# Kernel tuning notes

Hardware: AMD Instinct MI355X
Metric: run time of the kernel (lower is better)

The kernel has to match this reference:

```python
import jax, jax.numpy as jnp
import numpy as np

B, S, D, H, W = 2, 2048, 1024, 16, 128
HD = D // H


def setup_inputs() -> dict:
    key = jax.random.key(0)
    ks = jax.random.split(key, 9)
    s = 1.0 / np.sqrt(D)
    return {
        "x": jax.random.normal(ks[0], (B, S, D), jnp.float32),
        "Wq": jax.random.normal(ks[1], (D, D), jnp.float32) * s,
        "bq": jax.random.normal(ks[2], (D,), jnp.float32) * 0.01,
        "Wk": jax.random.normal(ks[3], (D, D), jnp.float32) * s,
        "bk": jax.random.normal(ks[4], (D,), jnp.float32) * 0.01,
        "Wv": jax.random.normal(ks[5], (D, D), jnp.float32) * s,
        "bv": jax.random.normal(ks[6], (D,), jnp.float32) * 0.01,
        "Wo": jax.random.normal(ks[7], (D, D), jnp.float32) * s,
        "bo": jax.random.normal(ks[8], (D,), jnp.float32) * 0.01,
    }


def reference(x, Wq, bq, Wk, bk, Wv, bv, Wo, bo):
    b, s, d = x.shape
    # projections (torch Linear: x @ W.T + b)
    q = (jnp.einsum('bsd,ed->bse', x, Wq) + bq).reshape(b, s, H, HD).transpose(0, 2, 1, 3)
    k = (jnp.einsum('bsd,ed->bse', x, Wk) + bk).reshape(b, s, H, HD).transpose(0, 2, 1, 3)
    v = (jnp.einsum('bsd,ed->bse', x, Wv) + bv).reshape(b, s, H, HD).transpose(0, 2, 1, 3)
    scores = jnp.einsum('bhqd,bhkd->bhqk', q, k) / jnp.sqrt(jnp.asarray(HD, x.dtype))
    # local band mask: mask[i, j] = 1 iff i - W//2 <= j <= i + W//2
    idx = jnp.arange(s)
    band = jnp.abs(idx[:, None] - idx[None, :]) <= (W // 2)  # [S, S]
    scores = jnp.where(band[None, None], scores, -jnp.inf)
    attn = jax.nn.softmax(scores, axis=-1)  # dropout is identity in eval
    ctx = jnp.einsum('bhqk,bhkd->bqhd', attn, v).reshape(b, s, d)
    out = jnp.einsum('bsd,ed->bse', ctx, Wo) + bo
    return out, attn
```

## Files before the change

### kernel.cpp

```cpp
#include <hip/hip_runtime.h>
#include <math.h>
#include <stdint.h>

typedef _Float16 f16;
typedef f16   f16x8 __attribute__((ext_vector_type(8)));
typedef f16   f16x4 __attribute__((ext_vector_type(4)));
typedef float f32x4 __attribute__((ext_vector_type(4)));

constexpr int Bc = 2, Sc = 2048, Dc = 1024, Hc = 16, HDc = 64;
constexpr size_t PROJ = (size_t)Bc * Sc * Dc;
constexpr size_t WN   = (size_t)Dc * Dc;

__device__ __forceinline__ void gload_lds16(const void* g, void* l) {
    unsigned int off = (unsigned int)(uintptr_t)l;
    auto lp = (__attribute__((address_space(3))) unsigned int*)(uintptr_t)off;
    auto gp = (const __attribute__((address_space(1))) unsigned int*)(uintptr_t)g;
    __builtin_amdgcn_global_load_lds(gp, lp, 16, 0, 0);
}

__device__ __forceinline__ void fill_rows32(float* __restrict__ attn, int grow0, int t) {
    const uint4 z = {0u, 0u, 0u, 0u};
    for (int rr = 0; rr < 32; ++rr) {
        const int gr = grow0 + rr;
        const int i = gr & (Sc - 1);
        const int lo = (i > 64) ? (i - 64) : 0;
        const int a0 = lo & ~31;
        const int hi = (i < Sc - 65) ? (i + 64) : (Sc - 1);
        int a1 = (hi + 32) & ~31; if (a1 > Sc) a1 = Sc;
        uint4* rowp = (uint4*)(attn + (size_t)gr * Sc);
        const int n4L = a0 >> 2;
        const int r0  = a1 >> 2;
        const int tot = n4L + (512 - r0);
        for (int idx = t; idx < tot; idx += 256) {
            const int p = (idx < n4L) ? idx : (r0 + idx - n4L);
            rowp[p] = z;
        }
    }
}

__global__ __launch_bounds__(256)
void pack_all(const float* __restrict__ x,
              const float* __restrict__ w0, const float* __restrict__ w1,
              const float* __restrict__ w2, const float* __restrict__ w3,
              f16* __restrict__ xd, f16* __restrict__ wd, f16* __restrict__ vT) {
    const int bid = blockIdx.x;
    if (bid == 8192) {
        const uint4 z = {0u, 0u, 0u, 0u};
        uint4* pre  = (uint4*)(vT - 256);
        uint4* post = (uint4*)(vT + (size_t)4 * 1024 * 1024);
        const int t = threadIdx.x;
        if (t < 32) pre[t] = z;
        else if (t < 64) post[t - 32] = z;
        return;
    }
    const float* src;
    f16* dst;
    int off4;
    if (bid < 4096) {
        src = x; dst = xd; off4 = bid;
    } else {
        const int wi = (bid - 4096) >> 10;
        const int r  = (bid - 4096) & 1023;
        src = (wi == 0) ? w0 : (wi == 1) ? w1 : (wi == 2) ? w2 : w3;
        dst = wd + (size_t)wi * WN;
        off4 = r;
    }
    const int i = off4 * 256 + threadIdx.x;
    float4 f = ((const float4*)src)[i];
    f16x4 h = {(f16)f.x, (f16)f.y, (f16)f.z, (f16)f.w};
    ((f16x4*)dst)[i] = h;
}

template <typename OutT, bool WITH_FILL>
__global__ __launch_bounds__(256, 3)
void gemm_mega(const f16* __restrict__ A, const f16* __restrict__ W,
               const float* __restrict__ b0, const float* __restrict__ b1,
               const float* __restrict__ b2,
               OutT* __restrict__ o0, OutT* __restrict__ o1, OutT* __restrict__ o2,
               float* __restrict__ fill, int n_ct) {
    constexpr int K = 1024, N = 1024;
    const int bid = blockIdx.x;
    const int t = threadIdx.x;

    int gid = bid;
    if (WITH_FILL) {
        const int g8 = bid >> 3, l8 = bid & 7;
        if (l8 < 3) {
            gid = g8 * 3 + l8;
        } else {
            fill_rows32(fill, (g8 * 5 + (l8 - 3)) * 32, t);
            return;
        }
    }

    __shared__ f16 sA[128 * 32];
    __shared__ f16 sB[128 * 32];

    const int w = t >> 6, l = t & 63, l15 = l & 15, quad = l >> 4;
    const int col_t = gid % n_ct, row_t = gid / n_ct;
    const int row0 = row_t * 128, col0 = col_t * 128;
    const int wr = w >> 1, wc = w & 1;

    f32x4 acc[4][4];
    #pragma unroll
    for (int i = 0; i < 4; ++i)
        #pragma unroll
        for (int j = 0; j < 4; ++j) acc[i][j] = (f32x4){0.f, 0.f, 0.f, 0.f};

    const int arow = t >> 2;
    const int koff = (t & 3) * 8;
    const f16* ga = A + (size_t)(row0 + arow) * K + koff;
    const f16* gb = W + (size_t)(col0 + arow) * K + koff;
    f16* lA1 = sA + w * 512;
    f16* lA2 = sA + 2048 + w * 512;
    f16* lB1 = sB + w * 512;
    f16* lB2 = sB + 2048 + w * 512;

    for (int k0 = 0; k0 < K; k0 += 32) {
        gload_lds16(ga + k0, lA1);
        gload_lds16(ga + (size_t)64 * K + k0, lA2);
        gload_lds16(gb + k0, lB1);
        gload_lds16(gb + (size_t)64 * K + k0, lB2);
        __syncthreads();

        f16x8 af[4], bf[4];
        #pragma unroll
        for (int mi = 0; mi < 4; ++mi)
            af[mi] = *(const f16x8*)&sA[(wr * 64 + mi * 16 + l15) * 32 + quad * 8];
        #pragma unroll
        for (int ni = 0; ni < 4; ++ni)
            bf[ni] = *(const f16x8*)&sB[(wc * 64 + ni * 16 + l15) * 32 + quad * 8];
        #pragma unroll
        for (int mi = 0; mi < 4; ++mi)
            #pragma unroll
            for (int ni = 0; ni < 4; ++ni)
                acc[mi][ni] = __builtin_amdgcn_mfma_f32_16x16x32_f16(af[mi], bf[ni], acc[mi][ni], 0, 0, 0);
        __syncthreads();
    }

    const int ten = col0 >> 10;
    const float* bias = (ten == 0) ? b0 : (ten == 1) ? b1 : b2;
    OutT* out = (ten == 0) ? o0 : (ten == 1) ? o1 : o2;
    const int nc0 = col0 & (N - 1);

    if constexpr (WITH_FILL) {
        if (ten == 2) {
            f16* vout = reinterpret_cast<f16*>(o2);
            #pragma unroll
            for (int mi = 0; mi < 4; ++mi)
                #pragma unroll
                for (int ni = 0; ni < 4; ++ni) {
                    const int tok  = row0 + wr * 64 + mi * 16 + quad * 4;
                    const int colv = nc0 + wc * 64 + ni * 16 + l15;
                    const float bvv = bias[colv];
                    f16x4 h4 = {(f16)(acc[mi][ni][0] + bvv), (f16)(acc[mi][ni][1] + bvv),
                                (f16)(acc[mi][ni][2] + bvv), (f16)(acc[mi][ni][3] + bvv)};
                    const int bb = tok >> 11;
                    *(f16x4*)&vout[((size_t)(bb * 1024 + colv)) * 2048 + (tok & 2047)] = h4;
                }
            return;
        }
    }

    #pragma unroll
    for (int mi = 0; mi < 4; ++mi)
        #pragma unroll
        for (int ni = 0; ni < 4; ++ni) {
            const int rbase = row0 + wr * 64 + mi * 16 + quad * 4;
            const int col = nc0 + wc * 64 + ni * 16 + l15;
            const float bv = bias[col];
            #pragma unroll
            for (int r = 0; r < 4; ++r)
                out[(size_t)(rbase + r) * N + col] = (OutT)(acc[mi][ni][r] + bv);
        }
}

__global__ __launch_bounds__(256, 3)
void gemm_o64(const f16* __restrict__ A, const f16* __restrict__ W,
              const float* __restrict__ bias, float* __restrict__ out) {
    constexpr int K = 1024, N = 1024;
    const int t = threadIdx.x;
    const int gid = blockIdx.x;

    __shared__ f16 sA[64 * 32];
    __shared__ f16 sB[128 * 32];

    const int w = t >> 6, l = t & 63, l15 = l & 15, quad = l >> 4;
    const int col_t = gid & 7, row_t = gid >> 3;
    const int row0 = row_t * 64, col0 = col_t * 128;

    f32x4 acc[4][2];
    #pragma unroll
    for (int i = 0; i < 4; ++i)
        #pragma unroll
        for (int j = 0; j < 2; ++j) acc[i][j] = (f32x4){0.f, 0.f, 0.f, 0.f};

    const int arow = t >> 2;
    const int koff = (t & 3) * 8;
    const f16* ga = A + (size_t)(row0 + arow) * K + koff;
    const f16* gb = W + (size_t)(col0 + arow) * K + koff;
    f16* lA1 = sA + w * 512;
    f16* lB1 = sB + w * 512;
    f16* lB2 = sB + 2048 + w * 512;

    for (int k0 = 0; k0 < K; k0 += 32) {
        gload_lds16(ga + k0, lA1);
        gload_lds16(gb + k0, lB1);
        gload_lds16(gb + (size_t)64 * K + k0, lB2);
        __syncthreads();

        f16x8 af[4], bf[2];
        #pragma unroll
        for (int mi = 0; mi < 4; ++mi)
            af[mi] = *(const f16x8*)&sA[(mi * 16 + l15) * 32 + quad * 8];
        #pragma unroll
        for (int ni = 0; ni < 2; ++ni)
            bf[ni] = *(const f16x8*)&sB[(w * 32 + ni * 16 + l15) * 32 + quad * 8];
        #pragma unroll
        for (int mi = 0; mi < 4; ++mi)
            #pragma unroll
            for (int ni = 0; ni < 2; ++ni)
                acc[mi][ni] = __builtin_amdgcn_mfma_f32_16x16x32_f16(af[mi], bf[ni], acc[mi][ni], 0, 0, 0);
        __syncthreads();
    }

    #pragma unroll
    for (int mi = 0; mi < 4; ++mi)
        #pragma unroll
        for (int ni = 0; ni < 2; ++ni) {
            const int rbase = row0 + mi * 16 + quad * 4;
            const int col = col0 + w * 32 + ni * 16 + l15;
            const float bv = bias[col];
            #pragma unroll
            for (int r = 0; r < 4; ++r)
                out[(size_t)(rbase + r) * N + col] = acc[mi][ni][r] + bv;
        }
}

__global__ __launch_bounds__(256, 3)
void attn_fused(const f16* __restrict__ qb, const f16* __restrict__ kb,
                const f16* __restrict__ vT, float* __restrict__ attn,
                f16* __restrict__ ctx) {
    const int bid = blockIdx.x;
    const int t = threadIdx.x;

    const int g7 = bid / 7, l7 = bid - g7 * 7;
    int aid;
    if (l7 < 4) {
        aid = g7 * 4 + l7;
    } else {
        fill_rows32(attn, 40960 + (g7 * 3 + (l7 - 4)) * 32, t);
        return;
    }

    __shared__ f16 sK[192 * 72];
    __shared__ f16 sVT[64 * 200];
    f16* sP = sK;

    const int w = t >> 6, l = t & 63, l15 = l & 15, quad = l >> 4;
    const int tile = aid & 31, h = (aid >> 5) & 15, b = aid >> 9;
    const int q0 = tile * 64;
    const int jbase = q0 - 64;

    const f16* qg2 = qb + ((size_t)(b * Sc + q0 + w * 16 + l15)) * Dc + h * HDc;
    const f16x8 aq0 = *(const f16x8*)&qg2[quad * 8];
    const f16x8 aq1 = *(const f16x8*)&qg2[32 + quad * 8];

    #pragma unroll
    for (int it = 0; it < 6; ++it) {
        const int idx = it * 256 + t;
        const int r = idx >> 3, c = (idx & 7) * 8;
        int j = jbase + r;
        j = (j < 0) ? 0 : (j > Sc - 1 ? Sc - 1 : j);
        const size_t goff = ((size_t)(b * Sc + j)) * Dc + h * HDc + c;
        *(uint4*)&sK[r * 72 + c] = *(const uint4*)&kb[goff];
    }
    {
        const f16* vrow = vT + ((size_t)((b * Hc + h) * HDc)) * Sc + jbase;
        const int dd = t >> 2;
        #pragma unroll
        for (int it = 0; it < 6; ++it) {
            const int ch = it * 4 + (t & 3);
            *(uint4*)&sVT[dd * 200 + ch * 8] = *(const uint4*)&vrow[(size_t)dd * Sc + ch * 8];
        }
    }
    __syncthreads();

    f32x4 s[12];
    #pragma unroll
    for (int nt = 0; nt < 12; ++nt) s[nt] = (f32x4){0.f, 0.f, 0.f, 0.f};
    #pragma unroll
    for (int nt = 0; nt < 12; ++nt) {
        const f16x8 bk0 = *(const f16x8*)&sK[(nt * 16 + l15) * 72 + quad * 8];
        s[nt] = __builtin_amdgcn_mfma_f32_16x16x32_f16(aq0, bk0, s[nt], 0, 0, 0);
    }
    #pragma unroll
    for (int nt = 0; nt < 12; ++nt) {
        const f16x8 bk1 = *(const f16x8*)&sK[(nt * 16 + l15) * 72 + 32 + quad * 8];
        s[nt] = __builtin_amdgcn_mfma_f32_16x16x32_f16(aq1, bk1, s[nt], 0, 0, 0);
    }

    float invr[4];
    #pragma unroll
    for (int r = 0; r < 4; ++r) {
        const int row = w * 16 + quad * 4 + r;
        const int lo = (row > 64 - q0) ? row : (64 - q0);
        const int hi2 = (row + 128 < 2111 - q0) ? (row + 128) : (2111 - q0);
        float m = -1e30f;
        #pragma unroll
        for (int nt = 0; nt < 12; ++nt) {
            const int jrel = nt * 16 + l15;
            const float v = s[nt][r] * 0.125f;
            if (jrel >= lo && jrel <= hi2) m = fmaxf(m, v);
        }
        #pragma unroll
        for (int k = 1; k < 16; k <<= 1) m = fmaxf(m, __shfl_xor(m, k, 64));
        float sum = 0.f;
        #pragma unroll
        for (int nt = 0; nt < 12; ++nt) {
            const int jrel = nt * 16 + l15;
            const float v = s[nt][r] * 0.125f;
            const float e = (jrel >= lo && jrel <= hi2) ? __expf(v - m) : 0.f;
            s[nt][r] = e;
            sum += e;
        }
        #pragma unroll
        for (int k = 1; k < 16; k <<= 1) sum += __shfl_xor(sum, k, 64);
        invr[r] = 1.f / sum;
    }
    __syncthreads();

    float* abase = attn + ((size_t)(b * Hc + h) * Sc) * Sc;
    #pragma unroll
    for (int r = 0; r < 4; ++r) {
        const int row = w * 16 + quad * 4 + r;
        const int i = q0 + row;
        const int lo0 = (i > 64) ? (i - 64) : 0;
        const int a0 = lo0 & ~31;
        const int hi0 = (i < Sc - 65) ? (i + 64) : (Sc - 1);
        int a1 = (hi0 + 32) & ~31; if (a1 > Sc) a1 = Sc;
        const int alo = a0 - jbase, ahi = a1 - jbase;
        #pragma unroll
        for (int nt = 0; nt < 12; ++nt) {
            const int jrel = nt * 16 + l15;
            const float p = s[nt][r] * invr[r];
            sP[row * 200 + jrel] = (f16)p;
            if (jrel >= alo && jrel < ahi)
                abase[(size_t)i * Sc + (jbase + jrel)] = p;
        }
    }
    __syncthreads();

    f32x4 o[4];
    #pragma unroll
    for (int dt = 0; dt < 4; ++dt) o[dt] = (f32x4){0.f, 0.f, 0.f, 0.f};
    #pragma unroll
    for (int ks = 0; ks < 6; ++ks) {
        const f16x8 ap = *(const f16x8*)&sP[(w * 16 + l15) * 200 + ks * 32 + quad * 8];
        #pragma unroll
        for (int dt = 0; dt < 4; ++dt) {
            const f16x8 bv = *(const f16x8*)&sVT[(dt * 16 + l15) * 200 + ks * 32 + quad * 8];
            o[dt] = __builtin_amdgcn_mfma_f32_16x16x32_f16(ap, bv, o[dt], 0, 0, 0);
        }
    }
    f16* cg = ctx + ((size_t)(b * Sc + q0)) * Dc + h * HDc;
    #pragma unroll
    for (int dt = 0; dt < 4; ++dt)
        #pragma unroll
        for (int r = 0; r < 4; ++r) {
            const int row = w * 16 + quad * 4 + r;
            cg[(size_t)row * Dc + dt * 16 + l15] = (f16)o[dt][r];
        }
}

extern "C" void kernel_launch(void* const* d_in, const int* in_sizes, int n_in,
                              void* d_out, int out_size, void* d_ws, size_t ws_size,
                              hipStream_t stream) {
    const float* x  = (const float*)d_in[0];
    const float* Wq = (const float*)d_in[1];
    const float* bq = (const float*)d_in[2];
    const float* Wk = (const float*)d_in[3];
    const float* bk = (const float*)d_in[4];
    const float* Wv = (const float*)d_in[5];
    const float* bv = (const float*)d_in[6];
    const float* Wo = (const float*)d_in[7];
    const float* bo = (const float*)d_in[8];

    float* out  = (float*)d_out;
    float* attn = out + PROJ;

    char* ws = (char*)d_ws;
    f16* Wcat  = (f16*)ws;
    f16* x_f16 = (f16*)(ws + (size_t)8  * 1024 * 1024);
    f16* q_f16 = (f16*)(ws + (size_t)16 * 1024 * 1024);
    f16* k_f16 = (f16*)(ws + (size_t)24 * 1024 * 1024);
    f16* c_f16 = (f16*)(ws + (size_t)40 * 1024 * 1024);
    f16* vT    = (f16*)(ws + (size_t)48 * 1024 * 1024 + 512);

    pack_all<<<dim3(8193), dim3(256), 0, stream>>>(x, Wq, Wk, Wv, Wo, x_f16, Wcat, vT);

    gemm_mega<f16, true><<<dim3(2048), dim3(256), 0, stream>>>(
        x_f16, Wcat, bq, bk, bv, q_f16, k_f16, vT, attn, 24);

    attn_fused<<<dim3(1792), dim3(256), 0, stream>>>(
        q_f16, k_f16, vT, attn, c_f16);

    gemm_o64<<<dim3(512), dim3(256), 0, stream>>>(
        c_f16, Wcat + 3 * WN, bo, out);
}
```

Baseline: 644.6 us.

## Double-buffer LDS tiles in projection GEMMs to overlap global loads with MFMA

Both the fused QKV projection GEMM and the output projection GEMM now keep two LDS buffers and prefetch the next K-slice with global_load_lds while the current slice is consumed by MFMA. Explicit vmcnt/lgkmcnt waits and raw s_barrier calls replace __syncthreads so the prefetch can stay in flight. This is meant to hide global-memory latency, at the cost of doubling LDS per block, which may reduce occupancy. It also relies on the hand-written waitcnt values matching the number of outstanding loads.

```diff
diff --git a/kernel.cpp b/kernel.cpp
--- a/kernel.cpp
+++ b/kernel.cpp
@@ -93,8 +93,8 @@
         }
     }
 
-    __shared__ f16 sA[128 * 32];
-    __shared__ f16 sB[128 * 32];
+    __shared__ f16 sA[2][128 * 32];
+    __shared__ f16 sB[2][128 * 32];
 
     const int w = t >> 6, l = t & 63, l15 = l & 15, quad = l >> 4;
     const int col_t = gid % n_ct, row_t = gid / n_ct;
@@ -111,31 +111,41 @@
     const int koff = (t & 3) * 8;
     const f16* ga = A + (size_t)(row0 + arow) * K + koff;
     const f16* gb = W + (size_t)(col0 + arow) * K + koff;
-    f16* lA1 = sA + w * 512;
-    f16* lA2 = sA + 2048 + w * 512;
-    f16* lB1 = sB + w * 512;
-    f16* lB2 = sB + 2048 + w * 512;
-
+
+    auto STAGE = [&](int buf, int k0) {
+        gload_lds16(ga + k0,                    &sA[buf][w * 512]);
+        gload_lds16(ga + (size_t)64 * K + k0,   &sA[buf][2048 + w * 512]);
+        gload_lds16(gb + k0,                    &sB[buf][w * 512]);
+        gload_lds16(gb + (size_t)64 * K + k0,   &sB[buf][2048 + w * 512]);
+    };
+
+    STAGE(0, 0);
+    int cur = 0;
     for (int k0 = 0; k0 < K; k0 += 32) {
-        gload_lds16(ga + k0, lA1);
-        gload_lds16(ga + (size_t)64 * K + k0, lA2);
-        gload_lds16(gb + k0, lB1);
-        gload_lds16(gb + (size_t)64 * K + k0, lB2);
-        __syncthreads();
+        if (k0 + 32 < K) {
+            STAGE(cur ^ 1, k0 + 32);
+            asm volatile("s_waitcnt vmcnt(4)" ::: "memory");
+        } else {
+            asm volatile("s_waitcnt vmcnt(0)" ::: "memory");
+        }
+        __builtin_amdgcn_s_barrier();
 
         f16x8 af[4], bf[4];
         #pragma unroll
         for (int mi = 0; mi < 4; ++mi)
-            af[mi] = *(const f16x8*)&sA[(wr * 64 + mi * 16 + l15) * 32 + quad * 8];
+            af[mi] = *(const f16x8*)&sA[cur][(wr * 64 + mi * 16 + l15) * 32 + quad * 8];
         #pragma unroll
         for (int ni = 0; ni < 4; ++ni)
-            bf[ni] = *(const f16x8*)&sB[(wc * 64 + ni * 16 + l15) * 32 + quad * 8];
+            bf[ni] = *(const f16x8*)&sB[cur][(wc * 64 + ni * 16 + l15) * 32 + quad * 8];
         #pragma unroll
         for (int mi = 0; mi < 4; ++mi)
             #pragma unroll
             for (int ni = 0; ni < 4; ++ni)
                 acc[mi][ni] = __builtin_amdgcn_mfma_f32_16x16x32_f16(af[mi], bf[ni], acc[mi][ni], 0, 0, 0);
-        __syncthreads();
+
+        asm volatile("s_waitcnt lgkmcnt(0)" ::: "memory");
+        __builtin_amdgcn_s_barrier();
+        cur ^= 1;
     }
 
     const int ten = col0 >> 10;
@@ -182,8 +192,8 @@
     const int t = threadIdx.x;
     const int gid = blockIdx.x;
 
-    __shared__ f16 sA[64 * 32];
-    __shared__ f16 sB[128 * 32];
+    __shared__ f16 sA[2][64 * 32];
+    __shared__ f16 sB[2][128 * 32];
 
     const int w = t >> 6, l = t & 63, l15 = l & 15, quad = l >> 4;
     const int col_t = gid & 7, row_t = gid >> 3;
@@ -199,29 +209,40 @@
     const int koff = (t & 3) * 8;
     const f16* ga = A + (size_t)(row0 + arow) * K + koff;
     const f16* gb = W + (size_t)(col0 + arow) * K + koff;
-    f16* lA1 = sA + w * 512;
-    f16* lB1 = sB + w * 512;
-    f16* lB2 = sB + 2048 + w * 512;
-
+
+    auto STAGE = [&](int buf, int k0) {
+        gload_lds16(ga + k0,                  &sA[buf][w * 512]);
+        gload_lds16(gb + k0,                  &sB[buf][w * 512]);
+        gload_lds16(gb + (size_t)64 * K + k0, &sB[buf][2048 + w * 512]);
+    };
+
+    STAGE(0, 0);
+    int cur = 0;
     for (int k0 = 0; k0 < K; k0 += 32) {
-        gload_lds16(ga + k0, lA1);
-        gload_lds16(gb + k0, lB1);
-        gload_lds16(gb + (size_t)64 * K + k0, lB2);
-        __syncthreads();
+        if (k0 + 32 < K) {
+            STAGE(cur ^ 1, k0 + 32);
+            asm volatile("s_waitcnt vmcnt(3)" ::: "memory");
+        } else {
+            asm volatile("s_waitcnt vmcnt(0)" ::: "memory");
+        }
+        __builtin_amdgcn_s_barrier();
 
         f16x8 af[4], bf[2];
         #pragma unroll
         for (int mi = 0; mi < 4; ++mi)
-            af[mi] = *(const f16x8*)&sA[(mi * 16 + l15) * 32 + quad * 8];
+            af[mi] = *(const f16x8*)&sA[cur][(mi * 16 + l15) * 32 + quad * 8];
         #pragma unroll
         for (int ni = 0; ni < 2; ++ni)
-            bf[ni] = *(const f16x8*)&sB[(w * 32 + ni * 16 + l15) * 32 + quad * 8];
+            bf[ni] = *(const f16x8*)&sB[cur][(w * 32 + ni * 16 + l15) * 32 + quad * 8];
         #pragma unroll
         for (int mi = 0; mi < 4; ++mi)
             #pragma unroll
             for (int ni = 0; ni < 2; ++ni)
                 acc[mi][ni] = __builtin_amdgcn_mfma_f32_16x16x32_f16(af[mi], bf[ni], acc[mi][ni], 0, 0, 0);
-        __syncthreads();
+
+        asm volatile("s_waitcnt lgkmcnt(0)" ::: "memory");
+        __builtin_amdgcn_s_barrier();
+        cur ^= 1;
     }
 
     #pragma unroll
```

After: 642.8 us. No clear change (-0.3%).
